# Optimization experiments

Measured on AMD Instinct MI355X. Metric: run time of the kernel, lower is better.

Reference implementation:

```python
import jax, jax.numpy as jnp
import numpy as np

B, E, N, D = 1024, 64, 32, 64  # batch, entities, sampled neighbors, dim


def setup_inputs() -> dict:
    key = jax.random.key(0)
    ks = jax.random.split(key, 6)
    return {
        "self_vectors": jax.random.normal(ks[0], (B, E, 1, D), dtype=jnp.float32),
        "neighbor_vectors": jax.random.normal(ks[1], (B, E, N, D), dtype=jnp.float32),
        "neighbor_relations": jax.random.normal(ks[2], (B, E, N, D), dtype=jnp.float32),
        "user_embeddings": jax.random.normal(ks[3], (B, D), dtype=jnp.float32),
        "W": jax.random.normal(ks[4], (D, 2 * D), dtype=jnp.float32) * (1.0 / np.sqrt(2 * D)),
        "b": jax.random.normal(ks[5], (D,), dtype=jnp.float32) * 0.01,
    }


def reference(self_vectors, neighbor_vectors, neighbor_relations, user_embeddings, W, b):
    # per-neighbor relation scores: (u . r) over dim -> [B, E, N]
    scores = jnp.einsum("bd,bend->ben", user_embeddings, neighbor_relations)
    p = jax.nn.softmax(scores, axis=-1)  # over neighbors
    # weighted neighbor sum -> [B, E, D]
    neighbors_agg = jnp.einsum("ben,bend->bed", p, neighbor_vectors)
    # 'concat' aggregator: cat(self, agg) on feature axis -> [B*E, 2D]
    sv = self_vectors.reshape(B, E, D)
    output = jnp.concatenate([sv, neighbors_agg], axis=-1).reshape(-1, 2 * D)
    output = output @ W.T + b  # Linear(2D -> D)
    return jax.nn.relu(output).reshape(B, -1, D)  # act = ReLU (inner KGCN layers)
```

## Files before the change

kernel.cpp:

```cpp
#include <hip/hip_runtime.h>
#include <math.h>

#define NB  1024
#define NE  64
#define NN  32
#define ND  64

__global__ __launch_bounds__(256) void kgcn_agg_kernel(
    const float* __restrict__ self_v,
    const float* __restrict__ nbr_v,
    const float* __restrict__ nbr_r,
    const float* __restrict__ user,
    const float* __restrict__ W,
    const float* __restrict__ bias,
    float* __restrict__ out)
{
    const int pair = blockIdx.x;
    const int b    = pair >> 6;
    const int t    = threadIdx.x;

    __shared__ float4 s_u4[16];
    __shared__ float4 s_x4[32];
    __shared__ float  s_scores[NN];
    __shared__ float  s_p[NN];
    __shared__ float4 s_part4[256];

    float* s_u    = (float*)s_u4;
    float* s_x    = (float*)s_x4;
    float* s_part = (float*)s_part4;

    if (t < 64) {
        s_u[t] = user[b * ND + t];
    } else if (t < 128) {
        s_x[t - 64] = self_v[(size_t)pair * ND + (t - 64)];
    }
    __syncthreads();

    const float4* rel4 = (const float4*)(nbr_r + (size_t)pair * (NN * ND));
    const float4* nv4  = (const float4*)(nbr_v + (size_t)pair * (NN * ND));

    const int col = t & 15;
    const int rg  = t >> 4;
    const int n_a = rg;
    const int n_b = rg + 16;

    float4 u4 = s_u4[col];

    float4 ra = rel4[t];
    float4 rb = rel4[t + 256];
    float4 va = nv4[t];
    float4 vb = nv4[t + 256];

    float pa = ra.x * u4.x + ra.y * u4.y + ra.z * u4.z + ra.w * u4.w;
    float pb = rb.x * u4.x + rb.y * u4.y + rb.z * u4.z + rb.w * u4.w;

    #pragma unroll
    for (int off = 8; off > 0; off >>= 1) {
        pa += __shfl_down(pa, off, 16);
        pb += __shfl_down(pb, off, 16);
    }
    if (col == 0) {
        s_scores[n_a] = pa;
        s_scores[n_b] = pb;
    }
    __syncthreads();

    if (t < 32) {
        float v = s_scores[t];
        float m = v;
        #pragma unroll
        for (int off = 16; off > 0; off >>= 1)
            m = fmaxf(m, __shfl_xor(m, off, 32));
        float e = __expf(v - m);
        float s = e;
        #pragma unroll
        for (int off = 16; off > 0; off >>= 1)
            s += __shfl_xor(s, off, 32);
        s_p[t] = e / s;
    }
    __syncthreads();

    float p_a = s_p[n_a];
    float p_b = s_p[n_b];
    float4 acc;
    acc.x = p_a * va.x + p_b * vb.x;
    acc.y = p_a * va.y + p_b * vb.y;
    acc.z = p_a * va.z + p_b * vb.z;
    acc.w = p_a * va.w + p_b * vb.w;
    s_part4[rg * 16 + col] = acc;
    __syncthreads();

    if (t < 64) {
        float a = 0.f;
        #pragma unroll
        for (int g = 0; g < 16; ++g)
            a += s_part[g * 64 + t];
        s_x[64 + t] = a;
    }
    __syncthreads();

    const int dout = t >> 2;
    const int q    = t & 3;
    const float4* W4 = (const float4*)W;
    float acc2 = 0.f;
    #pragma unroll
    for (int i = 0; i < 8; ++i) {
        float4 w = W4[dout * 32 + q * 8 + i];
        float4 x = s_x4[q * 8 + i];
        acc2 += w.x * x.x + w.y * x.y + w.z * x.z + w.w * x.w;
    }
    acc2 += __shfl_down(acc2, 2, 4);
    acc2 += __shfl_down(acc2, 1, 4);
    if (q == 0) {
        float r = acc2 + bias[dout];
        out[(size_t)pair * ND + dout] = fmaxf(r, 0.f);
    }
}

extern "C" void kernel_launch(void* const* d_in, const int* in_sizes, int n_in,
                              void* d_out, int out_size, void* d_ws, size_t ws_size,
                              hipStream_t stream) {
    const float* self_v = (const float*)d_in[0];
    const float* nbr_v  = (const float*)d_in[1];
    const float* nbr_r  = (const float*)d_in[2];
    const float* user   = (const float*)d_in[3];
    const float* W      = (const float*)d_in[4];
    const float* bias   = (const float*)d_in[5];
    float* out          = (float*)d_out;

    const int n_pairs = NB * NE;
    kgcn_agg_kernel<<<n_pairs, 256, 0, stream>>>(
        self_v, nbr_v, nbr_r, user, W, bias, out);
}
```

Baseline: 1.090 ms.

## Process multiple entity pairs per block with register-resident W and shuffle reductions

Each block now handles 16 (batch, entity) pairs in a loop instead of one, so the W matrix, bias and user vector are loaded into registers once per block and reused. Softmax probabilities are broadcast by wave shuffles instead of shared memory, and neighbor partial sums are reduced within the wave before a smaller shared-memory combine. Double-buffered shared arrays cut the barriers per pair. This lowers per-block launch and reload overhead but reduces the number of blocks and adds register pressure, which may limit memory-level parallelism on a bandwidth-bound kernel.

```diff
diff --git a/kernel.cpp b/kernel.cpp
--- a/kernel.cpp
+++ b/kernel.cpp
@@ -5,6 +5,7 @@
 #define NE  64
 #define NN  32
 #define ND  64
+#define PPB 16
 
 __global__ __launch_bounds__(256) void kgcn_agg_kernel(
     const float* __restrict__ self_v,
@@ -15,105 +16,121 @@
     const float* __restrict__ bias,
     float* __restrict__ out)
 {
-    const int pair = blockIdx.x;
-    const int b    = pair >> 6;
-    const int t    = threadIdx.x;
+    const int t     = threadIdx.x;
+    const int pair0 = blockIdx.x * PPB;
+    const int b     = pair0 >> 6;
 
-    __shared__ float4 s_u4[16];
-    __shared__ float4 s_x4[32];
-    __shared__ float  s_scores[NN];
-    __shared__ float  s_p[NN];
-    __shared__ float4 s_part4[256];
+    const int col  = t & 15;
+    const int rg   = t >> 4;
+    const int lane = t & 63;
+    const int wv   = t >> 6;
 
-    float* s_u    = (float*)s_u4;
-    float* s_x    = (float*)s_x4;
-    float* s_part = (float*)s_part4;
+    __shared__ float  s_scores[2][NN];
+    __shared__ float4 s_part4[2][64];
+    __shared__ float4 s_x4[2][36];
 
-    if (t < 64) {
-        s_u[t] = user[b * ND + t];
-    } else if (t < 128) {
-        s_x[t - 64] = self_v[(size_t)pair * ND + (t - 64)];
+    const float4 u4v = ((const float4*)(user + (size_t)b * ND))[col];
+    const float  bv  = bias[t >> 2];
+    float4 wr[8];
+    {
+        const float4* W4 = (const float4*)W;
+        #pragma unroll
+        for (int i = 0; i < 8; ++i)
+            wr[i] = W4[t * 8 + i];
     }
-    __syncthreads();
 
-    const float4* rel4 = (const float4*)(nbr_r + (size_t)pair * (NN * ND));
-    const float4* nv4  = (const float4*)(nbr_v + (size_t)pair * (NN * ND));
+    const float4* rel4 = (const float4*)(nbr_r + (size_t)pair0 * (NN * ND));
+    const float4* nv4  = (const float4*)(nbr_v + (size_t)pair0 * (NN * ND));
+    const float4* sv4  = (const float4*)(self_v + (size_t)pair0 * ND);
+    float* outp = out + (size_t)pair0 * ND;
 
-    const int col = t & 15;
-    const int rg  = t >> 4;
-    const int n_a = rg;
-    const int n_b = rg + 16;
+    #pragma unroll 1
+    for (int it = 0; it < PPB; ++it) {
+        const int buf  = it & 1;
+        const int base = it * 512;
 
-    float4 u4 = s_u4[col];
+        float4 ra = rel4[base + t];
+        float4 rb = rel4[base + t + 256];
+        float4 va = nv4[base + t];
+        float4 vb = nv4[base + t + 256];
+        float4 sv;
+        if (t < 16) sv = sv4[it * 16 + t];
 
-    float4 ra = rel4[t];
-    float4 rb = rel4[t + 256];
-    float4 va = nv4[t];
-    float4 vb = nv4[t + 256];
+        float pa = ra.x*u4v.x + ra.y*u4v.y + ra.z*u4v.z + ra.w*u4v.w;
+        float pb = rb.x*u4v.x + rb.y*u4v.y + rb.z*u4v.z + rb.w*u4v.w;
+        #pragma unroll
+        for (int off = 8; off > 0; off >>= 1) {
+            pa += __shfl_xor(pa, off, 16);
+            pb += __shfl_xor(pb, off, 16);
+        }
+        if (col == 0) {
+            s_scores[buf][rg]      = pa;
+            s_scores[buf][rg + 16] = pb;
+        }
+        if (t < 16) {
+            int c = t;
+            s_x4[buf][c + (c >> 3)] = sv;
+        }
+        __syncthreads();
 
-    float pa = ra.x * u4.x + ra.y * u4.y + ra.z * u4.z + ra.w * u4.w;
-    float pb = rb.x * u4.x + rb.y * u4.y + rb.z * u4.z + rb.w * u4.w;
-
-    #pragma unroll
-    for (int off = 8; off > 0; off >>= 1) {
-        pa += __shfl_down(pa, off, 16);
-        pb += __shfl_down(pb, off, 16);
-    }
-    if (col == 0) {
-        s_scores[n_a] = pa;
-        s_scores[n_b] = pb;
-    }
-    __syncthreads();
-
-    if (t < 32) {
-        float v = s_scores[t];
+        float v = s_scores[buf][t & 31];
         float m = v;
         #pragma unroll
         for (int off = 16; off > 0; off >>= 1)
             m = fmaxf(m, __shfl_xor(m, off, 32));
         float e = __expf(v - m);
-        float s = e;
+        float ssum = e;
         #pragma unroll
         for (int off = 16; off > 0; off >>= 1)
-            s += __shfl_xor(s, off, 32);
-        s_p[t] = e / s;
-    }
-    __syncthreads();
+            ssum += __shfl_xor(ssum, off, 32);
+        float rs  = __builtin_amdgcn_rcpf(ssum);
+        float p_a = __shfl(e, rg, 32) * rs;
+        float p_b = __shfl(e, rg + 16, 32) * rs;
 
-    float p_a = s_p[n_a];
-    float p_b = s_p[n_b];
-    float4 acc;
-    acc.x = p_a * va.x + p_b * vb.x;
-    acc.y = p_a * va.y + p_b * vb.y;
-    acc.z = p_a * va.z + p_b * vb.z;
-    acc.w = p_a * va.w + p_b * vb.w;
-    s_part4[rg * 16 + col] = acc;
-    __syncthreads();
+        float4 acc;
+        acc.x = p_a * va.x + p_b * vb.x;
+        acc.y = p_a * va.y + p_b * vb.y;
+        acc.z = p_a * va.z + p_b * vb.z;
+        acc.w = p_a * va.w + p_b * vb.w;
+        acc.x += __shfl_xor(acc.x, 16, 64);
+        acc.y += __shfl_xor(acc.y, 16, 64);
+        acc.z += __shfl_xor(acc.z, 16, 64);
+        acc.w += __shfl_xor(acc.w, 16, 64);
+        acc.x += __shfl_xor(acc.x, 32, 64);
+        acc.y += __shfl_xor(acc.y, 32, 64);
+        acc.z += __shfl_xor(acc.z, 32, 64);
+        acc.w += __shfl_xor(acc.w, 32, 64);
+        if (lane < 16) s_part4[buf][wv * 16 + lane] = acc;
+        __syncthreads();
 
-    if (t < 64) {
-        float a = 0.f;
+        if (t < 16) {
+            float4 a0 = s_part4[buf][t];
+            float4 a1 = s_part4[buf][16 + t];
+            float4 a2 = s_part4[buf][32 + t];
+            float4 a3 = s_part4[buf][48 + t];
+            float4 s;
+            s.x = (a0.x + a1.x) + (a2.x + a3.x);
+            s.y = (a0.y + a1.y) + (a2.y + a3.y);
+            s.z = (a0.z + a1.z) + (a2.z + a3.z);
+            s.w = (a0.w + a1.w) + (a2.w + a3.w);
+            int c = 16 + t;
+            s_x4[buf][c + (c >> 3)] = s;
+        }
+        __syncthreads();
+
+        const int q = t & 3;
+        float acc2 = 0.f;
         #pragma unroll
-        for (int g = 0; g < 16; ++g)
-            a += s_part[g * 64 + t];
-        s_x[64 + t] = a;
-    }
-    __syncthreads();
-
-    const int dout = t >> 2;
-    const int q    = t & 3;
-    const float4* W4 = (const float4*)W;
-    float acc2 = 0.f;
-    #pragma unroll
-    for (int i = 0; i < 8; ++i) {
-        float4 w = W4[dout * 32 + q * 8 + i];
-        float4 x = s_x4[q * 8 + i];
-        acc2 += w.x * x.x + w.y * x.y + w.z * x.z + w.w * x.w;
-    }
-    acc2 += __shfl_down(acc2, 2, 4);
-    acc2 += __shfl_down(acc2, 1, 4);
-    if (q == 0) {
-        float r = acc2 + bias[dout];
-        out[(size_t)pair * ND + dout] = fmaxf(r, 0.f);
+        for (int i = 0; i < 8; ++i) {
+            float4 x = s_x4[buf][q * 9 + i];
+            acc2 += wr[i].x * x.x + wr[i].y * x.y + wr[i].z * x.z + wr[i].w * x.w;
+        }
+        acc2 += __shfl_down(acc2, 2, 4);
+        acc2 += __shfl_down(acc2, 1, 4);
+        if (q == 0) {
+            float r = acc2 + bv;
+            outp[it * ND + (t >> 2)] = fmaxf(r, 0.f);
+        }
     }
 }
 
@@ -128,7 +145,7 @@
     const float* bias   = (const float*)d_in[5];
     float* out          = (float*)d_out;
 
-    const int n_pairs = NB * NE;
-    kgcn_agg_kernel<<<n_pairs, 256, 0, stream>>>(
+    const int n_blocks = (NB * NE) / PPB;
+    kgcn_agg_kernel<<<n_blocks, 256, 0, stream>>>(
         self_v, nbr_v, nbr_r, user, W, bias, out);
 }
```

Measured after the change: 992.2 us. -9.0%, faster.
